# Kernel tuning notes

Hardware: AMD Instinct MI355X
Metric: run time of the kernel (lower is better)

## Reference

```python
import jax, jax.numpy as jnp
import numpy as np

K = 14  # kernel_size == stride (non-overlapping patches)


def setup_inputs() -> dict:
    key = jax.random.key(0)
    k1, k2, k3, k4, k5 = jax.random.split(key, 5)
    b, c, h, w = 4, 384, 224, 224
    H, W = h // K, w // K  # final_size = (16, 16)
    hr_feats = jax.random.normal(k1, (b, c, h, w), dtype=jnp.float32)
    guidance = jnp.zeros((1,), dtype=jnp.float32)  # unused by forward()
    # attention_net: Dropout (eval=identity) -> Linear(dim, 1)
    attn_w = jax.random.normal(k2, (1, c), dtype=jnp.float32) * (1.0 / np.sqrt(c))
    attn_b = jnp.zeros((1,), dtype=jnp.float32)
    # learned per-position affine over the k*k patch axis
    w_kk = jnp.ones((K, K), dtype=jnp.float32) + 0.01 * jax.random.normal(k3, (K, K), dtype=jnp.float32)
    b_kk = jnp.zeros((K, K), dtype=jnp.float32) + 0.01 * jax.random.normal(k4, (K, K), dtype=jnp.float32)
    # forward-time dropout mask: torch.rand(b,H,W,1) > 0.2
    dropout_mask = jax.random.uniform(k5, (b, H, W, 1)) > 0.2
    return {"hr_feats": hr_feats, "guidance": guidance, "attn_w": attn_w,
            "attn_b": attn_b, "w_kk": w_kk, "b_kk": b_kk,
            "dropout_mask": dropout_mask}


def reference(hr_feats, guidance, attn_w, attn_b, w_kk, b_kk, dropout_mask):
    b, c, h, w = hr_feats.shape
    H, W = h // K, w // K
    # Unfold with stride == kernel_size: non-overlapping patches via reshape.
    # (b,c,h,w) -> (b,c,H,K,W,K) -> (b,H,W,K,K,c) -> (b,H,W,p=K*K,c)
    patches = hr_feats.reshape(b, c, H, K, W, K).transpose(0, 2, 4, 3, 5, 1)
    patches = patches.reshape(b, H, W, K * K, c)
    # tiny linear scorer: (b,H,W,p,c) @ (c,) -> (b,H,W,p)
    patch_logits = jnp.einsum('bhwpc,c->bhwp', patches, attn_w[0]) + attn_b[0]
    mask = dropout_mask.astype(patch_logits.dtype)  # (b,H,W,1)
    logits = patch_logits * mask * w_kk.reshape(-1) + b_kk.reshape(-1)
    attn = jax.nn.softmax(logits, axis=-1)  # over the p = K*K patch axis
    # softmax-weighted patch reduction
    downsampled = jnp.einsum('bhwpc,bhwp->bchw', patches, attn)
    return downsampled  # (b, c, H, W); slice [:, :c] is identity here
```

## Files before the change

kernel.cpp:

```cpp
#include <hip/hip_runtime.h>
#include <math.h>

#define B 4
#define C 384
#define HIN 224
#define WIN 224
#define KS 14
#define HB 16
#define WBL 16
#define P 196
#define HW (HIN * WIN)
#define CG 2
#define CPG (C / CG)
#define NT 49
#define NC 8

__global__ __launch_bounds__(256) void k_gemv(const float* __restrict__ hr,
                                              const float* __restrict__ attn_w,
                                              float* __restrict__ part) {
    __shared__ float wlds[CPG];
    const int tid = threadIdx.x;
    const int cg = blockIdx.x & 1;
    const int t  = (blockIdx.x >> 1) % NT;
    const int b  = blockIdx.x / (2 * NT);
    if (tid < CPG) wlds[tid] = attn_w[cg * CPG + tid];
    __syncthreads();

    const float* base = hr + (size_t)(b * C + cg * CPG) * HW + t * 1024 + tid * 4;
    float4 acc = make_float4(0.f, 0.f, 0.f, 0.f);
    #pragma unroll 8
    for (int c = 0; c < CPG; ++c) {
        const float4 v = *reinterpret_cast<const float4*>(base + (size_t)c * HW);
        const float wc = wlds[c];
        acc.x += v.x * wc; acc.y += v.y * wc; acc.z += v.z * wc; acc.w += v.w * wc;
    }
    reinterpret_cast<float4*>(part + (size_t)(b * CG + cg) * HW + t * 1024)[tid] = acc;
}

__global__ __launch_bounds__(256) void k_softmax(const float* __restrict__ part,
                                                 const float* __restrict__ attn_b,
                                                 const float* __restrict__ w_kk,
                                                 const float* __restrict__ b_kk,
                                                 const int* __restrict__ mask,
                                                 float* __restrict__ attn) {
    const int blk = blockIdx.x;
    const int wb = blk % WBL;
    const int hb = (blk / WBL) % HB;
    const int b = blk / (WBL * HB);
    const int tid = threadIdx.x;

    float logit = 0.f;
    float l = -INFINITY;
    if (tid < P) {
        const int ki = tid / KS, kj = tid % KS;
        const size_t idx = (size_t)(hb * KS + ki) * WIN + wb * KS + kj;
        const float rv = part[(size_t)(b * CG + 0) * HW + idx]
                       + part[(size_t)(b * CG + 1) * HW + idx];
        const float m = mask[(b * HB + hb) * WBL + wb] ? 1.f : 0.f;
        logit = (rv + attn_b[0]) * m * w_kk[tid] + b_kk[tid];
        l = logit;
    }

    __shared__ float smax[4], ssum[4];
    float v = l;
    #pragma unroll
    for (int off = 32; off; off >>= 1) v = fmaxf(v, __shfl_xor(v, off));
    if ((tid & 63) == 0) smax[tid >> 6] = v;
    __syncthreads();
    const float bm = fmaxf(fmaxf(smax[0], smax[1]), fmaxf(smax[2], smax[3]));

    float e = (tid < P) ? __expf(logit - bm) : 0.f;
    float s = e;
    #pragma unroll
    for (int off = 32; off; off >>= 1) s += __shfl_xor(s, off);
    if ((tid & 63) == 0) ssum[tid >> 6] = s;
    __syncthreads();
    const float bs = ssum[0] + ssum[1] + ssum[2] + ssum[3];

    if (tid < P) attn[(size_t)blk * P + tid] = e / bs;
}

__global__ __launch_bounds__(256) void k_weighted(const float* __restrict__ hr,
                                                  const float* __restrict__ attn,
                                                  float* __restrict__ out) {
    __shared__ float e_lds[KS * WIN];
    __shared__ float4 red4[224];
    __shared__ float colsum[WIN];
    const int tid = threadIdx.x;
    const int cg = blockIdx.x % 48;
    const int hb = (blockIdx.x / 48) & 15;
    const int b  = blockIdx.x / (48 * 16);

    const float* abase = attn + (size_t)((b * HB + hb) * WBL) * P;
    for (int i = tid; i < WBL * P; i += 256) {
        const int wb = i / P, p = i % P;
        e_lds[(p / KS) * WIN + wb * KS + (p % KS)] = abase[i];
    }
    __syncthreads();

    const int ki0 = tid / 56, fc = tid % 56;
    for (int n = 0; n < NC; ++n) {
        const int c = cg * NC + n;
        const float* hbase = hr + (size_t)((b * C + c) * HIN + hb * KS) * WIN;
        if (tid < 224) {
            float4 acc = make_float4(0.f, 0.f, 0.f, 0.f);
            #pragma unroll
            for (int r = ki0; r < KS; r += 4) {
                const float4 v = *reinterpret_cast<const float4*>(hbase + r * WIN + fc * 4);
                const float4 e = *reinterpret_cast<const float4*>(e_lds + r * WIN + fc * 4);
                acc.x += v.x * e.x; acc.y += v.y * e.y;
                acc.z += v.z * e.z; acc.w += v.w * e.w;
            }
            red4[tid] = acc;
        }
        __syncthreads();
        if (tid < 56) {
            const float4 a0 = red4[tid], a1 = red4[56 + tid],
                         a2 = red4[112 + tid], a3 = red4[168 + tid];
            reinterpret_cast<float4*>(colsum)[tid] = make_float4(
                a0.x + a1.x + a2.x + a3.x, a0.y + a1.y + a2.y + a3.y,
                a0.z + a1.z + a2.z + a3.z, a0.w + a1.w + a2.w + a3.w);
        }
        __syncthreads();
        if (tid < WBL) {
            float s = 0.f;
            #pragma unroll
            for (int kj = 0; kj < KS; ++kj) s += colsum[tid * KS + kj];
            out[(size_t)((b * C + c) * HB + hb) * WBL + tid] = s;
        }
    }
}

extern "C" void kernel_launch(void* const* d_in, const int* in_sizes, int n_in,
                              void* d_out, int out_size, void* d_ws, size_t ws_size,
                              hipStream_t stream) {
    const float* hr      = (const float*)d_in[0];
    const float* attn_w  = (const float*)d_in[2];
    const float* attn_b  = (const float*)d_in[3];
    const float* w_kk    = (const float*)d_in[4];
    const float* b_kk    = (const float*)d_in[5];
    const int*   mask    = (const int*)d_in[6];
    float* out = (float*)d_out;

    float* part = (float*)d_ws;
    float* attn = part + (size_t)B * CG * HW;

    k_gemv<<<B * NT * CG, 256, 0, stream>>>(hr, attn_w, part);
    k_softmax<<<B * HB * WBL, 256, 0, stream>>>(part, attn_b, w_kk, b_kk, mask, attn);
    k_weighted<<<B * 16 * 48, 256, 0, stream>>>(hr, attn, out);
}
```

Before: 109.5 us.

## Fuse softmax into the weighted-reduction kernel and drop per-channel block syncs

Removes the separate softmax kernel and its attention buffer. Each weighted-reduction block now rebuilds the logits for its row of patches from the GEMV partials into LDS, computes the exponentials and per-patch sums there, and divides by the sum only at the final output. The channel loop is also restructured so each wave handles two channels independently with scalar loads, replacing the block-wide barriers and shared reduction per channel. The trade-off is redundant softmax work: the part reads and exp computation are repeated in each of the 48 channel-group blocks sharing a patch row.

```diff
diff --git a/kernel.cpp b/kernel.cpp
--- a/kernel.cpp
+++ b/kernel.cpp
@@ -13,7 +13,6 @@
 #define CG 2
 #define CPG (C / CG)
 #define NT 49
-#define NC 8
 
 __global__ __launch_bounds__(256) void k_gemv(const float* __restrict__ hr,
                                               const float* __restrict__ attn_w,
@@ -37,96 +36,83 @@
     reinterpret_cast<float4*>(part + (size_t)(b * CG + cg) * HW + t * 1024)[tid] = acc;
 }
 
-__global__ __launch_bounds__(256) void k_softmax(const float* __restrict__ part,
-                                                 const float* __restrict__ attn_b,
-                                                 const float* __restrict__ w_kk,
-                                                 const float* __restrict__ b_kk,
-                                                 const int* __restrict__ mask,
-                                                 float* __restrict__ attn) {
-    const int blk = blockIdx.x;
-    const int wb = blk % WBL;
-    const int hb = (blk / WBL) % HB;
-    const int b = blk / (WBL * HB);
+__global__ __launch_bounds__(256) void k_fused3(const float* __restrict__ hr,
+                                                const float* __restrict__ part,
+                                                const float* __restrict__ attn_b,
+                                                const float* __restrict__ w_kk,
+                                                const float* __restrict__ b_kk,
+                                                const int* __restrict__ mask,
+                                                float* __restrict__ out) {
+    __shared__ float e_lds[KS * WIN];
+    __shared__ float wkk[P], bkk[P];
+    __shared__ float Swb[WBL], maskv[WBL];
+    __shared__ float colsum[4][WIN];
     const int tid = threadIdx.x;
-
-    float logit = 0.f;
-    float l = -INFINITY;
-    if (tid < P) {
-        const int ki = tid / KS, kj = tid % KS;
-        const size_t idx = (size_t)(hb * KS + ki) * WIN + wb * KS + kj;
-        const float rv = part[(size_t)(b * CG + 0) * HW + idx]
-                       + part[(size_t)(b * CG + 1) * HW + idx];
-        const float m = mask[(b * HB + hb) * WBL + wb] ? 1.f : 0.f;
-        logit = (rv + attn_b[0]) * m * w_kk[tid] + b_kk[tid];
-        l = logit;
-    }
-
-    __shared__ float smax[4], ssum[4];
-    float v = l;
-    #pragma unroll
-    for (int off = 32; off; off >>= 1) v = fmaxf(v, __shfl_xor(v, off));
-    if ((tid & 63) == 0) smax[tid >> 6] = v;
-    __syncthreads();
-    const float bm = fmaxf(fmaxf(smax[0], smax[1]), fmaxf(smax[2], smax[3]));
-
-    float e = (tid < P) ? __expf(logit - bm) : 0.f;
-    float s = e;
-    #pragma unroll
-    for (int off = 32; off; off >>= 1) s += __shfl_xor(s, off);
-    if ((tid & 63) == 0) ssum[tid >> 6] = s;
-    __syncthreads();
-    const float bs = ssum[0] + ssum[1] + ssum[2] + ssum[3];
-
-    if (tid < P) attn[(size_t)blk * P + tid] = e / bs;
-}
-
-__global__ __launch_bounds__(256) void k_weighted(const float* __restrict__ hr,
-                                                  const float* __restrict__ attn,
-                                                  float* __restrict__ out) {
-    __shared__ float e_lds[KS * WIN];
-    __shared__ float4 red4[224];
-    __shared__ float colsum[WIN];
-    const int tid = threadIdx.x;
+    const int wave = tid >> 6, lane = tid & 63;
     const int cg = blockIdx.x % 48;
     const int hb = (blockIdx.x / 48) & 15;
     const int b  = blockIdx.x / (48 * 16);
 
-    const float* abase = attn + (size_t)((b * HB + hb) * WBL) * P;
-    for (int i = tid; i < WBL * P; i += 256) {
-        const int wb = i / P, p = i % P;
-        e_lds[(p / KS) * WIN + wb * KS + (p % KS)] = abase[i];
+    if (tid < P) { wkk[tid] = w_kk[tid]; bkk[tid] = b_kk[tid]; }
+    if (tid >= 224 && tid < 240) maskv[tid - 224] = mask[(b * HB + hb) * WBL + (tid - 224)] ? 1.f : 0.f;
+    __syncthreads();
+
+    const float ab = attn_b[0];
+    const float* p0 = part + (size_t)(b * CG + 0) * HW + (size_t)(hb * KS) * WIN;
+    const float* p1 = part + (size_t)(b * CG + 1) * HW + (size_t)(hb * KS) * WIN;
+    for (int i = tid; i < KS * WIN; i += 256) {
+        const int ki = i / WIN, w = i % WIN;
+        const int wb = w / KS, kj = w - wb * KS;
+        const int p = ki * KS + kj;
+        const float rv = p0[i] + p1[i];
+        e_lds[i] = (rv + ab) * maskv[wb] * wkk[p] + bkk[p];
     }
     __syncthreads();
 
-    const int ki0 = tid / 56, fc = tid % 56;
-    for (int n = 0; n < NC; ++n) {
-        const int c = cg * NC + n;
-        const float* hbase = hr + (size_t)((b * C + c) * HIN + hb * KS) * WIN;
-        if (tid < 224) {
-            float4 acc = make_float4(0.f, 0.f, 0.f, 0.f);
-            #pragma unroll
-            for (int r = ki0; r < KS; r += 4) {
-                const float4 v = *reinterpret_cast<const float4*>(hbase + r * WIN + fc * 4);
-                const float4 e = *reinterpret_cast<const float4*>(e_lds + r * WIN + fc * 4);
-                acc.x += v.x * e.x; acc.y += v.y * e.y;
-                acc.z += v.z * e.z; acc.w += v.w * e.w;
-            }
-            red4[tid] = acc;
+    #pragma unroll
+    for (int wbi = 0; wbi < 4; ++wbi) {
+        const int wb = wave * 4 + wbi;
+        float m = -INFINITY;
+        for (int p = lane; p < P; p += 64)
+            m = fmaxf(m, e_lds[(p / KS) * WIN + wb * KS + (p % KS)]);
+        #pragma unroll
+        for (int off = 32; off; off >>= 1) m = fmaxf(m, __shfl_xor(m, off));
+        float s = 0.f;
+        for (int p = lane; p < P; p += 64) {
+            const int idx = (p / KS) * WIN + wb * KS + (p % KS);
+            const float e = __expf(e_lds[idx] - m);
+            e_lds[idx] = e;
+            s += e;
         }
-        __syncthreads();
-        if (tid < 56) {
-            const float4 a0 = red4[tid], a1 = red4[56 + tid],
-                         a2 = red4[112 + tid], a3 = red4[168 + tid];
-            reinterpret_cast<float4*>(colsum)[tid] = make_float4(
-                a0.x + a1.x + a2.x + a3.x, a0.y + a1.y + a2.y + a3.y,
-                a0.z + a1.z + a2.z + a3.z, a0.w + a1.w + a2.w + a3.w);
+        #pragma unroll
+        for (int off = 32; off; off >>= 1) s += __shfl_xor(s, off);
+        if (lane == 0) Swb[wb] = s;
+    }
+    __syncthreads();
+
+    #pragma unroll
+    for (int cc = 0; cc < 2; ++cc) {
+        const int c = cg * 8 + wave * 2 + cc;
+        const float* hbase = hr + ((size_t)(b * C + c) * HIN + hb * KS) * WIN;
+        float a0 = 0.f, a1 = 0.f, a2 = 0.f, a3 = 0.f;
+        #pragma unroll
+        for (int ki = 0; ki < KS; ++ki) {
+            const float* hrow = hbase + (size_t)ki * WIN;
+            const float* erow = e_lds + ki * WIN;
+            a0 += hrow[lane]       * erow[lane];
+            a1 += hrow[lane + 64]  * erow[lane + 64];
+            a2 += hrow[lane + 128] * erow[lane + 128];
+            if (lane < 32) a3 += hrow[lane + 192] * erow[lane + 192];
         }
-        __syncthreads();
-        if (tid < WBL) {
+        colsum[wave][lane] = a0;
+        colsum[wave][lane + 64] = a1;
+        colsum[wave][lane + 128] = a2;
+        if (lane < 32) colsum[wave][lane + 192] = a3;
+        if (lane < WBL) {
             float s = 0.f;
             #pragma unroll
-            for (int kj = 0; kj < KS; ++kj) s += colsum[tid * KS + kj];
-            out[(size_t)((b * C + c) * HB + hb) * WBL + tid] = s;
+            for (int k = 0; k < KS; ++k) s += colsum[wave][lane * KS + k];
+            out[((size_t)(b * C + c) * HB + hb) * WBL + lane] = s / Swb[lane];
         }
     }
 }
@@ -143,9 +129,7 @@
     float* out = (float*)d_out;
 
     float* part = (float*)d_ws;
-    float* attn = part + (size_t)B * CG * HW;
 
     k_gemv<<<B * NT * CG, 256, 0, stream>>>(hr, attn_w, part);
-    k_softmax<<<B * HB * WBL, 256, 0, stream>>>(part, attn_b, w_kk, b_kk, mask, attn);
-    k_weighted<<<B * 16 * 48, 256, 0, stream>>>(hr, attn, out);
+    k_fused3<<<B * 16 * 48, 256, 0, stream>>>(hr, part, attn_b, w_kk, b_kk, mask, out);
 }
```

Result: slower. 134.0 us (+22.3%).
